# Performance work log

Hardware: AMD Instinct MI355X
Metric: run time of the kernel (lower is better)

Reference implementation:

```python
import jax, jax.numpy as jnp
import numpy as np

EPS = 1e-5
NUM_HEADS = 3


def _ln(x, g, b):
    m = jnp.mean(x, axis=-1, keepdims=True)
    v = jnp.mean((x - m) ** 2, axis=-1, keepdims=True)
    return (x - m) * jax.lax.rsqrt(v + EPS) * g + b


def setup_inputs() -> dict:
    key = jax.random.key(0)
    ks = jax.random.split(key, 8)
    Bn, N, C = 256, 197, 192           # graph nodes, tokens per node, embed_dim
    E = 1024                           # edges
    hid = int(C * 4.0)                 # mlp hidden
    def w(k, shape, fan_in):
        return (jax.random.normal(k, shape, jnp.float32) / np.sqrt(fan_in)).astype(jnp.float32)
    return {
        "x": jax.random.normal(ks[0], (Bn, N, C), jnp.float32),
        "egde": jax.random.randint(ks[1], (2, E), 0, Bn),
        "norm1_g": jnp.ones((C,), jnp.float32),
        "norm1_b": jnp.zeros((C,), jnp.float32),
        "qkv_w": w(ks[2], (3 * C, C), C),          # Linear(dim, 3*dim, bias=False)
        "proj_w": w(ks[3], (C, C), C),
        "proj_b": jnp.zeros((C,), jnp.float32),
        "norm2_g": jnp.ones((C,), jnp.float32),
        "norm2_b": jnp.zeros((C,), jnp.float32),
        "fc1_w": w(ks[4], (hid, C), C),
        "fc1_b": jnp.zeros((hid,), jnp.float32),
        "fc2_w": w(ks[5], (C, hid), hid),
        "fc2_b": jnp.zeros((C,), jnp.float32),
    }


def reference(x, egde, norm1_g, norm1_b, qkv_w, proj_w, proj_b,
              norm2_g, norm2_b, fc1_w, fc1_b, fc2_w, fc2_b):
    Bn, N, C = x.shape
    H = NUM_HEADS
    hd = C // H
    scale = hd ** -0.5

    # --- MEConv2 ---
    xn = _ln(x, norm1_g, norm1_b)
    qkv = (xn @ qkv_w.T).reshape(Bn, N, 3, H, hd)
    src, dst = egde[0], egde[1]        # x_j = source, aggregation index = target
    xi = qkv[dst]                      # [E, N, 3, H, hd]
    xj = qkv[src]
    q = xi[:, :, 0]                    # [E, N, H, hd] (from destination)
    v = xi[:, :, 2]                    # note: v comes from x_i, as in the source
    k = xj[:, :, 1]                    # key from source node
    attn = jnp.einsum('enhd,emhd->ehnm', q, k) * scale   # [E, H, N, N]
    attn = jax.nn.softmax(attn, axis=-1)
    msg = jnp.einsum('ehnm,emhd->enhd', attn, v).reshape(-1, N, C)
    msg = msg @ proj_w.T + proj_b      # [E, N, C]
    # scatter-mean over destination nodes (empty nodes -> 0, like torch scatter)
    agg = jax.ops.segment_sum(msg, dst, num_segments=Bn)
    cnt = jax.ops.segment_sum(jnp.ones(dst.shape, x.dtype), dst, num_segments=Bn)
    y = agg / jnp.maximum(cnt, 1.0)[:, None, None]

    # --- residual + MLP ---
    x = x + y
    h = _ln(x, norm2_g, norm2_b)
    h = jax.nn.gelu(h @ fc1_w.T + fc1_b, approximate=False)  # torch nn.GELU = exact
    h = h @ fc2_w.T + fc2_b
    return x + h
```

## Files before the change

kernel.cpp:

```cpp
#include <hip/hip_runtime.h>
#include <hip/hip_bf16.h>
#include <cstddef>


typedef __attribute__((ext_vector_type(8))) short bf8_t;
typedef __attribute__((ext_vector_type(4))) float f4_t;

#define GLOBAL_AS __attribute__((address_space(1)))
#define LDS_AS    __attribute__((address_space(3)))

__device__ __forceinline__ float bf2f(unsigned short u) {
  union { unsigned int i; float f; } x; x.i = ((unsigned int)u) << 16; return x.f;
}
__device__ __forceinline__ unsigned short f2bf(float f) {
  unsigned int u = __builtin_bit_cast(unsigned int, f);
  u = (u + 0x7FFFu + ((u >> 16) & 1u)) >> 16;
  return (unsigned short)u;
}
__device__ __forceinline__ unsigned int cvt_pk_bf16(float a, float b) {
  unsigned int r;
  asm("v_cvt_pk_bf16_f32 %0, %1, %2" : "=v"(r) : "v"(a), "v"(b));
  return r;
}
__device__ __forceinline__ void gload16(const unsigned short* g, unsigned short* l) {
  __builtin_amdgcn_global_load_lds((const GLOBAL_AS unsigned int*)g,
                                   (LDS_AS unsigned int*)l, 16, 0, 0);
}

__global__ __launch_bounds__(256) void wcvt_kernel(
    const float* __restrict__ qkvw, const float* __restrict__ projw,
    const float* __restrict__ fc1w, const float* __restrict__ fc2w,
    unsigned short* __restrict__ dst) {
  int i = blockIdx.x * 256 + threadIdx.x;
  float v;
  if (i < 110592)      v = qkvw[i];
  else if (i < 147456) v = projw[i - 110592];
  else if (i < 294912) v = fc1w[i - 147456];
  else                 v = fc2w[i - 294912];
  dst[i] = f2bf(v);
}

__global__ __launch_bounds__(256) void ln_bf16_kernel(const float* __restrict__ X,
    const float* __restrict__ g, const float* __restrict__ b,
    unsigned short* __restrict__ Y) {
  int row = blockIdx.x * 4 + (threadIdx.x >> 6);
  int lane = threadIdx.x & 63;
  const float* xr = X + (size_t)row * 192;
  float v0 = xr[lane], v1 = xr[lane + 64], v2 = xr[lane + 128];
  float s = v0 + v1 + v2, ss = v0 * v0 + v1 * v1 + v2 * v2;
#pragma unroll
  for (int o = 32; o > 0; o >>= 1) { s += __shfl_xor(s, o, 64); ss += __shfl_xor(ss, o, 64); }
  float mean = s * (1.f / 192.f);
  float var = ss * (1.f / 192.f) - mean * mean;
  float r = rsqrtf(var + 1e-5f);
  unsigned short* yr = Y + (size_t)row * 192;
  yr[lane]       = f2bf((v0 - mean) * r * g[lane]       + b[lane]);
  yr[lane + 64]  = f2bf((v1 - mean) * r * g[lane + 64]  + b[lane + 64]);
  yr[lane + 128] = f2bf((v2 - mean) * r * g[lane + 128] + b[lane + 128]);
}

template<int MODE, int NK>
__global__ __launch_bounds__(256) void gemm_bf16(
    const unsigned short* __restrict__ A, const unsigned short* __restrict__ W,
    const float* __restrict__ bias, const float* __restrict__ xres,
    const int* __restrict__ cntg, void* __restrict__ Cout,
    unsigned short* __restrict__ Cvt, int ldc) {
  constexpr int LDA = 208;
  __shared__ unsigned short As[128 * LDA];
  __shared__ unsigned short Ws[64 * LDA];
  const int tid = threadIdx.x;
  const int m0 = blockIdx.x * 128, n0 = blockIdx.y * 64;
  const int wave = tid >> 6, lane = tid & 63;
  const int mfrag = lane & 15, quad = lane >> 4;
  const int K = NK * 192;

  f4_t acc[2][4];
#pragma unroll
  for (int i = 0; i < 2; ++i)
#pragma unroll
    for (int j = 0; j < 4; ++j) acc[i][j] = (f4_t){0.f, 0.f, 0.f, 0.f};

  for (int kc = 0; kc < NK; ++kc) {
    __syncthreads();
    for (int it = wave; it < 78; it += 4) {
      if (it < 52) {
        int idx = it * 64 + lane;
        int r = idx / 26, c = idx % 26;
        int c8 = min(c * 8, 184);
        gload16(A + (size_t)(m0 + r) * K + kc * 192 + c8, As + it * 512);
      } else {
        int idx = (it - 52) * 64 + lane;
        int r = idx / 26, c = idx % 26;
        int c8 = min(c * 8, 184);
        gload16(W + (size_t)(n0 + r) * K + kc * 192 + c8, Ws + (it - 52) * 512);
      }
    }
    __syncthreads();
#pragma unroll
    for (int ks = 0; ks < 6; ++ks) {
      bf8_t a0 = *(const bf8_t*)(As + (wave * 32 + mfrag) * LDA + ks * 32 + quad * 8);
      bf8_t a1 = *(const bf8_t*)(As + (wave * 32 + 16 + mfrag) * LDA + ks * 32 + quad * 8);
#pragma unroll
      for (int nt = 0; nt < 4; ++nt) {
        bf8_t bf = *(const bf8_t*)(Ws + (nt * 16 + mfrag) * LDA + ks * 32 + quad * 8);
        acc[0][nt] = __builtin_amdgcn_mfma_f32_16x16x32_bf16(a0, bf, acc[0][nt], 0, 0, 0);
        acc[1][nt] = __builtin_amdgcn_mfma_f32_16x16x32_bf16(a1, bf, acc[1][nt], 0, 0, 0);
      }
    }
  }

#pragma unroll
  for (int mt = 0; mt < 2; ++mt)
#pragma unroll
    for (int nt = 0; nt < 4; ++nt)
#pragma unroll
      for (int reg = 0; reg < 4; ++reg) {
        int row = m0 + wave * 32 + mt * 16 + quad * 4 + reg;
        int col = n0 + nt * 16 + mfrag;
        float v = acc[mt][nt][reg];
        if constexpr (MODE == 0) {
          if (col < 384) {
            ((unsigned short*)Cout)[(size_t)row * 384 + col] = f2bf(v);
          } else {
            int cc = col - 384, hh = cc >> 6, dd = cc & 63;
            int bb = row / 197, tt = row - bb * 197;
            Cvt[((size_t)(bb * 3 + hh) * 64 + dd) * 200 + tt] = f2bf(v);
          }
        }
      }
}

__global__ __launch_bounds__(256) void mlp_kernel(
    const unsigned short* __restrict__ xn,
    const unsigned short* __restrict__ wfc1,
    const unsigned short* __restrict__ wfc2,
    const float* __restrict__ b1, const float* __restrict__ b2,
    float* __restrict__ outF) {
  __shared__ unsigned short As[64 * 208];
  __shared__ unsigned short WF[13824];
  __shared__ unsigned short Hs[64 * 72];
  const int tid = threadIdx.x;
  const int m0 = blockIdx.x * 64;
  const int wave = tid >> 6, lane = tid & 63;
  const int mfrag = lane & 15, quad = lane >> 4;

  for (int it = wave; it < 26; it += 4) {
    int idx = it * 64 + lane;
    int r = idx / 26, c = idx % 26;
    int c8 = min(c * 8, 184);
    gload16(xn + (size_t)(m0 + r) * 192 + c8, As + it * 512);
  }

  f4_t acc2[12];
#pragma unroll
  for (int j = 0; j < 12; ++j) acc2[j] = (f4_t){0.f, 0.f, 0.f, 0.f};

  for (int hc = 0; hc < 12; ++hc) {
    __syncthreads();
    for (int it = wave; it < 26; it += 4) {
      int idx = it * 64 + lane;
      int r = idx / 26, c = idx % 26;
      int c8 = min(c * 8, 184);
      gload16(wfc1 + (size_t)(hc * 64 + r) * 192 + c8, WF + it * 512);
    }
    __syncthreads();

    f4_t acc1[4];
#pragma unroll
    for (int j = 0; j < 4; ++j) acc1[j] = (f4_t){0.f, 0.f, 0.f, 0.f};
#pragma unroll
    for (int ks = 0; ks < 6; ++ks) {
      bf8_t a0 = *(const bf8_t*)(As + (wave * 16 + mfrag) * 208 + ks * 32 + quad * 8);
#pragma unroll
      for (int nt = 0; nt < 4; ++nt) {
        bf8_t bf = *(const bf8_t*)(WF + (nt * 16 + mfrag) * 208 + ks * 32 + quad * 8);
        acc1[nt] = __builtin_amdgcn_mfma_f32_16x16x32_bf16(a0, bf, acc1[nt], 0, 0, 0);
      }
    }
#pragma unroll
    for (int nt = 0; nt < 4; ++nt) {
      float bb = b1[hc * 64 + nt * 16 + mfrag];
#pragma unroll
      for (int reg = 0; reg < 4; ++reg) {
        float v = acc1[nt][reg] + bb;
        v = 0.5f * v * (1.f + erff(v * 0.70710678118654752f));
        Hs[(wave * 16 + quad * 4 + reg) * 72 + nt * 16 + mfrag] = f2bf(v);
      }
    }

    __syncthreads();
    for (int it = wave; it < 27; it += 4) {
      int idx = it * 64 + lane;
      int r = idx / 9, sg = idx % 9;
      int sg8 = min(sg * 8, 56);
      gload16(wfc2 + (size_t)r * 768 + hc * 64 + sg8, WF + it * 512);
    }
    __syncthreads();

#pragma unroll
    for (int ks = 0; ks < 2; ++ks) {
      bf8_t a0 = *(const bf8_t*)(Hs + (wave * 16 + mfrag) * 72 + ks * 32 + quad * 8);
#pragma unroll
      for (int nt = 0; nt < 12; ++nt) {
        bf8_t bf = *(const bf8_t*)(WF + (nt * 16 + mfrag) * 72 + ks * 32 + quad * 8);
        acc2[nt] = __builtin_amdgcn_mfma_f32_16x16x32_bf16(a0, bf, acc2[nt], 0, 0, 0);
      }
    }
  }

#pragma unroll
  for (int nt = 0; nt < 12; ++nt) {
    float bb = b2[nt * 16 + mfrag];
#pragma unroll
    for (int reg = 0; reg < 4; ++reg) {
      int row = m0 + wave * 16 + quad * 4 + reg;
      int col = nt * 16 + mfrag;
      float v = acc2[nt][reg] + bb + outF[(size_t)row * 192 + col];
      outF[(size_t)row * 192 + col] = v;
    }
  }
}

__global__ __launch_bounds__(256) void proj_ln_kernel(
    const unsigned short* __restrict__ A,
    const unsigned short* __restrict__ W,
    const float* __restrict__ bias,
    const float* __restrict__ xres,
    const int* __restrict__ cntg,
    const float* __restrict__ g2, const float* __restrict__ b2,
    float* __restrict__ outF,
    unsigned short* __restrict__ xnout) {
  constexpr int LDA = 208;
  __shared__ unsigned short As[128 * LDA];
  __shared__ unsigned short Ws[64 * LDA];
  const int tid = threadIdx.x;
  const int m0 = blockIdx.x * 128;
  const int wave = tid >> 6, lane = tid & 63;
  const int mfrag = lane & 15, quad = lane >> 4;

  f4_t acc[3][2][4];
#pragma unroll
  for (int nc = 0; nc < 3; ++nc)
#pragma unroll
    for (int i = 0; i < 2; ++i)
#pragma unroll
      for (int j = 0; j < 4; ++j) acc[nc][i][j] = (f4_t){0.f, 0.f, 0.f, 0.f};

  for (int it = wave; it < 52; it += 4) {
    int idx = it * 64 + lane;
    int r = idx / 26, c = idx % 26;
    int c8 = min(c * 8, 184);
    gload16(A + (size_t)(m0 + r) * 192 + c8, As + it * 512);
  }

  for (int nc = 0; nc < 3; ++nc) {
    if (nc > 0) __syncthreads();
    for (int it = wave; it < 26; it += 4) {
      int idx = it * 64 + lane;
      int r = idx / 26, c = idx % 26;
      int c8 = min(c * 8, 184);
      gload16(W + (size_t)(nc * 64 + r) * 192 + c8, Ws + it * 512);
    }
    __syncthreads();
#pragma unroll
    for (int ks = 0; ks < 6; ++ks) {
      bf8_t a0 = *(const bf8_t*)(As + (wave * 32 + mfrag) * LDA + ks * 32 + quad * 8);
      bf8_t a1 = *(const bf8_t*)(As + (wave * 32 + 16 + mfrag) * LDA + ks * 32 + quad * 8);
#pragma unroll
      for (int nt = 0; nt < 4; ++nt) {
        bf8_t bf = *(const bf8_t*)(Ws + (nt * 16 + mfrag) * LDA + ks * 32 + quad * 8);
        acc[nc][0][nt] = __builtin_amdgcn_mfma_f32_16x16x32_bf16(a0, bf, acc[nc][0][nt], 0, 0, 0);
        acc[nc][1][nt] = __builtin_amdgcn_mfma_f32_16x16x32_bf16(a1, bf, acc[nc][1][nt], 0, 0, 0);
      }
    }
  }

  float pb[12], pg[12], pbb[12];
#pragma unroll
  for (int nc = 0; nc < 3; ++nc)
#pragma unroll
    for (int nt = 0; nt < 4; ++nt) {
      int col = nc * 64 + nt * 16 + mfrag;
      pb[nc * 4 + nt] = bias[col];
      pg[nc * 4 + nt] = g2[col];
      pbb[nc * 4 + nt] = b2[col];
    }

#pragma unroll
  for (int mt = 0; mt < 2; ++mt)
#pragma unroll
    for (int reg = 0; reg < 4; ++reg) {
      const int row = m0 + wave * 32 + mt * 16 + quad * 4 + reg;
      const int cn = cntg[row / 197];
      const float rc = (cn > 0) ? 1.f / (float)cn : 0.f;
      float vv[12];
      float s = 0.f, ss = 0.f;
#pragma unroll
      for (int nc = 0; nc < 3; ++nc)
#pragma unroll
        for (int nt = 0; nt < 4; ++nt) {
          int col = nc * 64 + nt * 16 + mfrag;
          float v = (cn > 0) ? acc[nc][mt][nt][reg] * rc + pb[nc * 4 + nt] : 0.f;
          v += xres[(size_t)row * 192 + col];
          vv[nc * 4 + nt] = v;
          s += v;
          ss += v * v;
        }
#pragma unroll
      for (int off = 1; off < 16; off <<= 1) {
        s += __shfl_xor(s, off, 64);
        ss += __shfl_xor(ss, off, 64);
      }
      const float mean = s * (1.f / 192.f);
      const float var = ss * (1.f / 192.f) - mean * mean;
      const float r = rsqrtf(var + 1e-5f);
#pragma unroll
      for (int nc = 0; nc < 3; ++nc)
#pragma unroll
        for (int nt = 0; nt < 4; ++nt) {
          int col = nc * 64 + nt * 16 + mfrag;
          float v = vv[nc * 4 + nt];
          outF[(size_t)row * 192 + col] = v;
          xnout[(size_t)row * 192 + col] =
              f2bf((v - mean) * r * pg[nc * 4 + nt] + pbb[nc * 4 + nt]);
        }
    }
}

__global__ __launch_bounds__(512) void attnA_kernel(
    const unsigned short* __restrict__ qk, const unsigned short* __restrict__ vtg,
    const int* __restrict__ edge, unsigned short* __restrict__ msgbuf) {
  const int e = blockIdx.x, h = blockIdx.y;
  const int s = edge[e], b = edge[1024 + e];
  __shared__ unsigned short Ks[208 * 72];
  __shared__ unsigned short Vt[64 * 232];
  __shared__ unsigned short Ps[8][640];
  const int tid = threadIdx.x;
  const int wave = tid >> 6, lane = tid & 63;
  const int mfrag = lane & 15, quad = lane >> 4;

  for (int i = tid; i < 197 * 8; i += 512) {
    int m = i >> 3, c8 = i & 7;
    *(float4*)(Ks + m * 72 + c8 * 8) =
        *(const float4*)(qk + (size_t)(s * 197 + m) * 384 + 192 + h * 64 + c8 * 8);
  }
  for (int i = tid; i < 64 * 25; i += 512) {
    int d = i / 25, c8 = i - d * 25;
    *(float4*)(Vt + d * 232 + c8 * 8) =
        *(const float4*)(vtg + ((size_t)(b * 3 + h) * 64 + d) * 200 + c8 * 8);
  }
  __syncthreads();
  for (int i = tid; i < 64 * 35; i += 512) {
    int d = i / 35, kk = 197 + (i - d * 35);
    Vt[d * 232 + kk] = 0;
  }
  __syncthreads();

  for (int st = wave; st < 13; st += 8) {
    const int m0 = st * 16;
    const size_t qrow = (size_t)(b * 197 + min(m0 + mfrag, 196)) * 384 + h * 64;
    bf8_t a0 = *(const bf8_t*)(qk + qrow + quad * 8);
    bf8_t a1 = *(const bf8_t*)(qk + qrow + 32 + quad * 8);

    f4_t S[13];
#pragma unroll
    for (int nt = 0; nt < 13; ++nt) {
      bf8_t k0 = *(const bf8_t*)(Ks + (nt * 16 + mfrag) * 72 + quad * 8);
      bf8_t k1 = *(const bf8_t*)(Ks + (nt * 16 + mfrag) * 72 + 32 + quad * 8);
      f4_t z = (f4_t){0.f, 0.f, 0.f, 0.f};
      z = __builtin_amdgcn_mfma_f32_16x16x32_bf16(a0, k0, z, 0, 0, 0);
      S[nt] = __builtin_amdgcn_mfma_f32_16x16x32_bf16(a1, k1, z, 0, 0, 0);
    }

#pragma unroll
    for (int reg = 0; reg < 4; ++reg)
      S[12][reg] = (mfrag < 5) ? S[12][reg] : -1e30f;

    float mx[4] = {-1e30f, -1e30f, -1e30f, -1e30f};
#pragma unroll
    for (int nt = 0; nt < 13; ++nt)
#pragma unroll
      for (int reg = 0; reg < 4; ++reg) mx[reg] = fmaxf(mx[reg], S[nt][reg]);
#pragma unroll
    for (int off = 1; off < 16; off <<= 1)
#pragma unroll
      for (int reg = 0; reg < 4; ++reg) mx[reg] = fmaxf(mx[reg], __shfl_xor(mx[reg], off, 64));

    constexpr float CEXP = 0.18033688011112042f;
    float sum[4] = {0.f, 0.f, 0.f, 0.f};
#pragma unroll
    for (int nt = 0; nt < 13; ++nt)
#pragma unroll
      for (int reg = 0; reg < 4; ++reg) {
        float p = exp2f((S[nt][reg] - mx[reg]) * CEXP);
        S[nt][reg] = p;
        sum[reg] += p;
      }
#pragma unroll
    for (int off = 1; off < 16; off <<= 1)
#pragma unroll
      for (int reg = 0; reg < 4; ++reg) sum[reg] += __shfl_xor(sum[reg], off, 64);
    float inv[4];
#pragma unroll
    for (int reg = 0; reg < 4; ++reg) inv[reg] = __builtin_amdgcn_rcpf(sum[reg]);

    f4_t o[4];
#pragma unroll
    for (int dt = 0; dt < 4; ++dt) o[dt] = (f4_t){0.f, 0.f, 0.f, 0.f};
    unsigned short* buf = Ps[wave];
#pragma unroll
    for (int kt = 0; kt < 7; ++kt) {
#pragma unroll
      for (int reg = 0; reg < 4; ++reg) {
        float p0 = S[kt * 2][reg];
        float p1 = (kt * 2 + 1 < 13) ? S[kt * 2 + 1][reg] : 0.f;
        unsigned int u = cvt_pk_bf16(p0, p1);
        buf[(quad * 4 + reg) * 40 + mfrag]      = (unsigned short)u;
        buf[(quad * 4 + reg) * 40 + 16 + mfrag] = (unsigned short)(u >> 16);
      }
      bf8_t pf = *(const bf8_t*)(buf + mfrag * 40 + quad * 8);
#pragma unroll
      for (int dt = 0; dt < 4; ++dt) {
        bf8_t vf = *(const bf8_t*)(Vt + (dt * 16 + mfrag) * 232 + kt * 32 + quad * 8);
        o[dt] = __builtin_amdgcn_mfma_f32_16x16x32_bf16(pf, vf, o[dt], 0, 0, 0);
      }
    }

#pragma unroll
    for (int dt = 0; dt < 4; dt += 2)
#pragma unroll
      for (int reg = 0; reg < 4; ++reg) {
        int q = m0 + quad * 4 + reg;
        unsigned int u = cvt_pk_bf16(o[dt][reg] * inv[reg], o[dt + 1][reg] * inv[reg]);
        if (q < 197) {
          size_t base = (size_t)e * 37824 + q * 192 + h * 64 + dt * 16 + mfrag;
          msgbuf[base]      = (unsigned short)u;
          msgbuf[base + 16] = (unsigned short)(u >> 16);
        }
      }
  }
}

__global__ __launch_bounds__(256) void aggregate_kernel(
    const unsigned short* __restrict__ msgbuf, const int* __restrict__ edge,
    unsigned short* __restrict__ agg, int* __restrict__ cntg) {
  const int b = blockIdx.x, chunk = blockIdx.y;
  __shared__ int list[1024];
  __shared__ int lc;
  const int tid = threadIdx.x;
  if (tid == 0) lc = 0;
  __syncthreads();
  for (int e = tid; e < 1024; e += 256)
    if (edge[1024 + e] == b) { int p = atomicAdd(&lc, 1); list[p] = e; }
  __syncthreads();
  const int cnt = lc;
  if (chunk == 0 && tid == 0) cntg[b] = cnt;
  const int base = chunk * 9456;
  for (int i8 = tid; i8 < 1182; i8 += 256) {
    int i = base + i8 * 8;
    float sum[8];
#pragma unroll
    for (int kk = 0; kk < 8; ++kk) sum[kk] = 0.f;
    for (int j = 0; j < cnt; ++j) {
      float4 t = *(const float4*)(msgbuf + (size_t)list[j] * 37824 + i);
      const unsigned short* u = (const unsigned short*)&t;
#pragma unroll
      for (int kk = 0; kk < 8; ++kk) sum[kk] += bf2f(u[kk]);
    }
    unsigned short o[8];
#pragma unroll
    for (int kk = 0; kk < 8; ++kk) o[kk] = f2bf(sum[kk]);
    *(float4*)(agg + (size_t)b * 37824 + i) = *(const float4*)o;
  }
}

extern "C" void kernel_launch(void* const* d_in, const int* in_sizes, int n_in,
                              void* d_out, int out_size, void* d_ws, size_t ws_size,
                              hipStream_t stream) {
  const float* x      = (const float*)d_in[0];
  const int*   edge   = (const int*)d_in[1];
  const float* n1g    = (const float*)d_in[2];
  const float* n1b    = (const float*)d_in[3];
  const float* qkv_w  = (const float*)d_in[4];
  const float* proj_w = (const float*)d_in[5];
  const float* proj_b = (const float*)d_in[6];
  const float* n2g    = (const float*)d_in[7];
  const float* n2b    = (const float*)d_in[8];
  const float* fc1_w  = (const float*)d_in[9];
  const float* fc1_b  = (const float*)d_in[10];
  const float* fc2_w  = (const float*)d_in[11];
  const float* fc2_b  = (const float*)d_in[12];
  float* out = (float*)d_out;

  char* ws = (char*)d_ws;
  unsigned short* msgbuf = (unsigned short*)ws;
  unsigned short* qk     = (unsigned short*)(ws + 77463552);
  unsigned short* xn     = (unsigned short*)(ws + 116195328);
  unsigned short* agg    = (unsigned short*)(ws + 135561216);
  unsigned short* vtg    = (unsigned short*)(ws + 154927104);
  unsigned short* wqkv   = (unsigned short*)(ws + 174587904);
  unsigned short* wproj  = (unsigned short*)(ws + 174809088);
  unsigned short* wfc1   = (unsigned short*)(ws + 174882816);
  unsigned short* wfc2   = (unsigned short*)(ws + 175177728);
  int*            cntg   = (int*)           (ws + 175472640);

  dim3 blk(256);
  wcvt_kernel<<<dim3(1728), blk, 0, stream>>>(qkv_w, proj_w, fc1_w, fc2_w, wqkv);

  ln_bf16_kernel<<<dim3(12608), blk, 0, stream>>>(x, n1g, n1b, xn);
  gemm_bf16<0, 1><<<dim3(394, 9), blk, 0, stream>>>(xn, wqkv, nullptr, nullptr, nullptr, qk, vtg, 384);
  attnA_kernel<<<dim3(1024, 3), dim3(512), 0, stream>>>(qk, vtg, edge, msgbuf);
  aggregate_kernel<<<dim3(256, 4), blk, 0, stream>>>(msgbuf, edge, agg, cntg);
  proj_ln_kernel<<<dim3(394), blk, 0, stream>>>(agg, wproj, proj_b, x, cntg, n2g, n2b, out, xn);
  mlp_kernel<<<dim3(788), blk, 0, stream>>>(xn, wfc1, wfc2, fc1_b, fc2_b, out);
}
```

Measured before the change: 426.4 us.

## Read MLP weights straight from global memory and drop block-wide LDS staging

The MLP kernel no longer stages the activation tile and the fc1/fc2 weight tiles through shared memory with block-wide barriers. Each wave keeps its 16-row activation fragment in registers, reads weight fragments directly from global memory (expecting cache hits across blocks), and uses a small per-wave LDS buffer only for the GELU output. Launch bounds now request 4 blocks per CU, trading LDS reuse of weights for less shared memory, no __syncthreads, and higher occupancy. The cost is many more uncoalesced 16-byte global loads per wave, since each wave fetches the full weight matrices itself.

```diff
diff --git a/kernel.cpp b/kernel.cpp
--- a/kernel.cpp
+++ b/kernel.cpp
@@ -130,51 +130,40 @@
       }
 }
 
-__global__ __launch_bounds__(256) void mlp_kernel(
+__global__ __launch_bounds__(256, 4) void mlp_kernel(
     const unsigned short* __restrict__ xn,
     const unsigned short* __restrict__ wfc1,
     const unsigned short* __restrict__ wfc2,
     const float* __restrict__ b1, const float* __restrict__ b2,
     float* __restrict__ outF) {
-  __shared__ unsigned short As[64 * 208];
-  __shared__ unsigned short WF[13824];
-  __shared__ unsigned short Hs[64 * 72];
+  __shared__ unsigned short Hs[4][16 * 72];
   const int tid = threadIdx.x;
   const int m0 = blockIdx.x * 64;
   const int wave = tid >> 6, lane = tid & 63;
   const int mfrag = lane & 15, quad = lane >> 4;
-
-  for (int it = wave; it < 26; it += 4) {
-    int idx = it * 64 + lane;
-    int r = idx / 26, c = idx % 26;
-    int c8 = min(c * 8, 184);
-    gload16(xn + (size_t)(m0 + r) * 192 + c8, As + it * 512);
-  }
+  unsigned short* hbuf = Hs[wave];
+
+  const unsigned short* arow = xn + (size_t)(m0 + wave * 16 + mfrag) * 192 + quad * 8;
+  bf8_t aA[6];
+#pragma unroll
+  for (int ks = 0; ks < 6; ++ks) aA[ks] = *(const bf8_t*)(arow + ks * 32);
 
   f4_t acc2[12];
 #pragma unroll
   for (int j = 0; j < 12; ++j) acc2[j] = (f4_t){0.f, 0.f, 0.f, 0.f};
 
   for (int hc = 0; hc < 12; ++hc) {
-    __syncthreads();
-    for (int it = wave; it < 26; it += 4) {
-      int idx = it * 64 + lane;
-      int r = idx / 26, c = idx % 26;
-      int c8 = min(c * 8, 184);
-      gload16(wfc1 + (size_t)(hc * 64 + r) * 192 + c8, WF + it * 512);
-    }
-    __syncthreads();
-
     f4_t acc1[4];
 #pragma unroll
     for (int j = 0; j < 4; ++j) acc1[j] = (f4_t){0.f, 0.f, 0.f, 0.f};
 #pragma unroll
-    for (int ks = 0; ks < 6; ++ks) {
-      bf8_t a0 = *(const bf8_t*)(As + (wave * 16 + mfrag) * 208 + ks * 32 + quad * 8);
-#pragma unroll
-      for (int nt = 0; nt < 4; ++nt) {
-        bf8_t bf = *(const bf8_t*)(WF + (nt * 16 + mfrag) * 208 + ks * 32 + quad * 8);
-        acc1[nt] = __builtin_amdgcn_mfma_f32_16x16x32_bf16(a0, bf, acc1[nt], 0, 0, 0);
+    for (int nt = 0; nt < 4; ++nt) {
+      const unsigned short* w1row =
+          wfc1 + (size_t)(hc * 64 + nt * 16 + mfrag) * 192 + quad * 8;
+#pragma unroll
+      for (int ks = 0; ks < 6; ++ks) {
+        bf8_t bf = *(const bf8_t*)(w1row + ks * 32);
+        acc1[nt] = __builtin_amdgcn_mfma_f32_16x16x32_bf16(aA[ks], bf, acc1[nt], 0, 0, 0);
       }
     }
 #pragma unroll
@@ -184,26 +173,17 @@
       for (int reg = 0; reg < 4; ++reg) {
         float v = acc1[nt][reg] + bb;
         v = 0.5f * v * (1.f + erff(v * 0.70710678118654752f));
-        Hs[(wave * 16 + quad * 4 + reg) * 72 + nt * 16 + mfrag] = f2bf(v);
-      }
-    }
-
-    __syncthreads();
-    for (int it = wave; it < 27; it += 4) {
-      int idx = it * 64 + lane;
-      int r = idx / 9, sg = idx % 9;
-      int sg8 = min(sg * 8, 56);
-      gload16(wfc2 + (size_t)r * 768 + hc * 64 + sg8, WF + it * 512);
-    }
-    __syncthreads();
-
-#pragma unroll
-    for (int ks = 0; ks < 2; ++ks) {
-      bf8_t a0 = *(const bf8_t*)(Hs + (wave * 16 + mfrag) * 72 + ks * 32 + quad * 8);
+        hbuf[(quad * 4 + reg) * 72 + nt * 16 + mfrag] = f2bf(v);
+      }
+    }
+#pragma unroll
+    for (int ks2 = 0; ks2 < 2; ++ks2) {
+      bf8_t a2 = *(const bf8_t*)(hbuf + mfrag * 72 + ks2 * 32 + quad * 8);
 #pragma unroll
       for (int nt = 0; nt < 12; ++nt) {
-        bf8_t bf = *(const bf8_t*)(WF + (nt * 16 + mfrag) * 72 + ks * 32 + quad * 8);
-        acc2[nt] = __builtin_amdgcn_mfma_f32_16x16x32_bf16(a0, bf, acc2[nt], 0, 0, 0);
+        bf8_t bf = *(const bf8_t*)(wfc2 + (size_t)(nt * 16 + mfrag) * 768 +
+                                   hc * 64 + ks2 * 32 + quad * 8);
+        acc2[nt] = __builtin_amdgcn_mfma_f32_16x16x32_bf16(a2, bf, acc2[nt], 0, 0, 0);
       }
     }
   }
```

Measured after the change: 567.3 us. 33.0% more time.
